# Kernel optimization log

Hardware: AMD Instinct MI355X
Metric: run time of the kernel (lower is better)

The kernel has to match this reference:

```python
import jax, jax.numpy as jnp
import numpy as np

H = 768   # hidden_size
E = 9     # num_entity_types
R = 10    # num_relation_types
B, S, N = 8, 4096, 64
P = N * (N - 1) // 2  # 2016 ordered pairs i<j


def setup_inputs() -> dict:
    key = jax.random.key(0)
    ks = jax.random.split(key, 10)
    sd = 0.02
    return {
        "sequence_output": jax.random.normal(ks[0], (B, S, H), jnp.float32),
        "attention_mask": jnp.ones((B, S), jnp.int32),
        "entity_spans": jnp.sort(jax.random.randint(ks[1], (B, N, 2), 0, S), axis=-1),
        # entity_classifier: Linear(H, H//2) -> ReLU -> Linear(H//2, E)
        "w1": jax.random.normal(ks[2], (H, H // 2), jnp.float32) * sd,
        "b1": jnp.zeros((H // 2,), jnp.float32),
        "w2": jax.random.normal(ks[3], (H // 2, E), jnp.float32) * sd,
        "b2": jnp.zeros((E,), jnp.float32),
        # relation_classifier: Linear(2H, H) -> ReLU -> Linear(H, R)
        "rw1": jax.random.normal(ks[4], (2 * H, H), jnp.float32) * sd,
        "rb1": jnp.zeros((H,), jnp.float32),
        "rw2": jax.random.normal(ks[5], (H, R), jnp.float32) * sd,
        "rb2": jnp.zeros((R,), jnp.float32),
    }


def reference(sequence_output, attention_mask, entity_spans,
              w1, b1, w2, b2, rw1, rb1, rw2, rb2):
    # entity classifier over all tokens (dropout is identity in eval)
    h = jax.nn.relu(jnp.einsum('bsh,hf->bsf', sequence_output, w1) + b1)
    entity_logits = jnp.einsum('bsf,fe->bse', h, w2) + b2  # [B,S,E]

    # span mean-pooling via a [B,N,S] membership mask (segment-mean)
    pos = jnp.arange(S)
    start = entity_spans[..., 0:1]  # [B,N,1]
    end = entity_spans[..., 1:2]    # [B,N,1]
    mask = ((pos >= start) & (pos < end)).astype(sequence_output.dtype)  # [B,N,S]
    counts = jnp.clip(mask.sum(-1, keepdims=True), 1.0)  # avoid /0 for empty spans
    entity_reprs = jnp.einsum('bns,bsh->bnh', mask, sequence_output) / counts  # [B,N,H]
    pooled_logits = jnp.einsum('bns,bse->bne', mask, entity_logits) / counts   # [B,N,E]
    entity_types = jnp.argmax(pooled_logits, axis=-1)  # [B,N]

    # all i<j pairs, batched relation classifier (replaces per-pair Python loop)
    ii, jj = np.triu_indices(N, k=1)  # static index sets, len P
    pair = jnp.concatenate([entity_reprs[:, ii], entity_reprs[:, jj]], axis=-1)  # [B,P,2H]
    rh = jax.nn.relu(jnp.einsum('bpk,kh->bph', pair, rw1) + rb1)
    relation_logits = jnp.einsum('bph,hr->bpr', rh, rw2) + rb2  # [B,P,R]
    relation_types = jnp.argmax(relation_logits, axis=-1)  # [B,P]

    return entity_logits, relation_logits, entity_reprs, entity_types, relation_types
```

## Files before the change

kernel.cpp:

```cpp
#include <hip/hip_runtime.h>
#include <hip/hip_bf16.h>

#define Hh 768
#define Ff 384
#define Ee 9
#define Rr 10
#define Bb 8
#define Ss 4096
#define Nn_ENT 64
#define Pp 2016
#define CH 16
#define NC 256

typedef short bf16x8 __attribute__((ext_vector_type(8)));
typedef float f32x4 __attribute__((ext_vector_type(4)));

__device__ __forceinline__ void async_copy16(void* lds, const void* g) {
  auto* l = (__attribute__((address_space(3))) unsigned int*)(lds);
  auto* p = (const __attribute__((address_space(1))) unsigned int*)(g);
  __builtin_amdgcn_global_load_lds(p, l, 16, 0, 0);
}

__global__ __launch_bounds__(256) void transpose_w1(const float* __restrict__ w1,
                                                    unsigned short* __restrict__ wt) {
  __shared__ unsigned short tile[64][65];
  const int bk = blockIdx.x * 64;
  const int bc = blockIdx.y * 64;
  const int c = threadIdx.x & 63, kq = threadIdx.x >> 6;
#pragma unroll
  for (int i = 0; i < 16; ++i) {
    int k = kq * 16 + i;
    float v = w1[(size_t)(bk + k) * Ff + bc + c];
    tile[c][k] = __bfloat16_as_ushort(__float2bfloat16(v));
  }
  __syncthreads();
  const int k2 = threadIdx.x & 63, cq = threadIdx.x >> 6;
#pragma unroll
  for (int i = 0; i < 16; ++i) {
    int c2 = cq * 16 + i;
    wt[(size_t)(bc + c2) * Hh + bk + k2] = tile[c2][k2];
  }
}

__global__ __launch_bounds__(192) void seq_prep(const float* __restrict__ seq,
                                                unsigned short* __restrict__ seq16,
                                                float* __restrict__ Pc) {
  const int c = blockIdx.x, b = blockIdx.y;
  const int t = threadIdx.x;
  const size_t base = ((size_t)b * Ss + (size_t)c * CH) * Hh;
  const float4* p = (const float4*)(seq + base) + t;
  ushort4* q = (ushort4*)(seq16 + base) + t;
  float4 acc = {0.f, 0.f, 0.f, 0.f};
#pragma unroll
  for (int s = 0; s < CH; ++s) {
    float4 v = p[(size_t)s * (Hh / 4)];
    acc.x += v.x; acc.y += v.y; acc.z += v.z; acc.w += v.w;
    ushort4 o;
    o.x = __bfloat16_as_ushort(__float2bfloat16(v.x));
    o.y = __bfloat16_as_ushort(__float2bfloat16(v.y));
    o.z = __bfloat16_as_ushort(__float2bfloat16(v.z));
    o.w = __bfloat16_as_ushort(__float2bfloat16(v.w));
    q[(size_t)s * (Hh / 4)] = o;
  }
  ((float4*)(Pc + ((size_t)b * NC + c) * Hh))[t] = acc;
}

__global__ __launch_bounds__(256) void gemm1_mfma(const unsigned short* __restrict__ A,
                                                  const unsigned short* __restrict__ Wt,
                                                  const float* __restrict__ b1,
                                                  unsigned short* __restrict__ H) {
  __shared__ unsigned short As[128 * 64];
  __shared__ unsigned short Bs[128 * 64];
  const int wg = blockIdx.x;
  const int lin = (wg & 7) * 96 + (wg >> 3);
  const int mt = lin / 3, nt = lin % 3;
  const int row0 = mt * 128, col0 = nt * 128;
  const int t = threadIdx.x;
  const int wid = t >> 6, lane = t & 63;
  const int wm = wid >> 1, wn = wid & 1;
  const int fr = lane & 15, fq = lane >> 4;
  const int srow = lane >> 3, scol = (lane & 7) * 8;
  const unsigned short* aA = A + (size_t)row0 * Hh;
  const unsigned short* aB = Wt + (size_t)col0 * Hh;

  f32x4 acc[4][4] = {};

  for (int ks = 0; ks < Hh / 64; ++ks) {
    const int k0 = ks * 64;
#pragma unroll
    for (int i = 0; i < 4; ++i) {
      const int r = (wid * 4 + i) * 8 + srow;
      async_copy16(&As[(wid * 4 + i) * 512], aA + (size_t)r * Hh + k0 + scol);
      async_copy16(&Bs[(wid * 4 + i) * 512], aB + (size_t)r * Hh + k0 + scol);
    }
    __syncthreads();
#pragma unroll
    for (int kk = 0; kk < 2; ++kk) {
      bf16x8 af[4], bfr[4];
#pragma unroll
      for (int m = 0; m < 4; ++m)
        af[m] = *(const bf16x8*)&As[(wm * 64 + m * 16 + fr) * 64 + kk * 32 + fq * 8];
#pragma unroll
      for (int n = 0; n < 4; ++n)
        bfr[n] = *(const bf16x8*)&Bs[(wn * 64 + n * 16 + fr) * 64 + kk * 32 + fq * 8];
#pragma unroll
      for (int m = 0; m < 4; ++m)
#pragma unroll
        for (int n = 0; n < 4; ++n)
          acc[m][n] = __builtin_amdgcn_mfma_f32_16x16x32_bf16(af[m], bfr[n], acc[m][n], 0, 0, 0);
    }
    if (ks < Hh / 64 - 1) __syncthreads();
  }

#pragma unroll
  for (int n = 0; n < 4; ++n) {
    const int col = col0 + wn * 64 + n * 16 + fr;
    const float bias = b1[col];
#pragma unroll
    for (int m = 0; m < 4; ++m) {
      const int rbase = row0 + wm * 64 + m * 16 + fq * 4;
#pragma unroll
      for (int j = 0; j < 4; ++j) {
        float x = fmaxf(acc[m][n][j] + bias, 0.f);
        H[(size_t)(rbase + j) * Ff + col] = __bfloat16_as_ushort(__float2bfloat16(x));
      }
    }
  }
}

__global__ __launch_bounds__(256) void gemm_uv_splitk(const float* __restrict__ A,
                                                      const float* __restrict__ rw1,
                                                      float* __restrict__ part) {
  const int uv = blockIdx.z & 1, ks = blockIdx.z >> 1;
  const float* Wp = rw1 + (size_t)uv * Hh * Hh + (size_t)ks * 192 * Hh;
  __shared__ float Ast[16][68];
  __shared__ float Wst[16][68];
  const int t = threadIdx.x;
  const int row0 = blockIdx.x * 64, col0 = blockIdx.y * 64;
  const int tm = (t & 15) * 4, tn = (t >> 4) * 4;
  const int lr = t >> 2, lk = (t & 3) * 4;
  const int wk = t >> 4, wc = (t & 15) * 4;
  float acc[4][4] = {};
  const float* Arow = A + (size_t)(row0 + lr) * Hh + ks * 192 + lk;
  for (int k0 = 0; k0 < 192; k0 += 16) {
    float4 av = *(const float4*)(Arow + k0);
    Ast[lk + 0][lr] = av.x; Ast[lk + 1][lr] = av.y;
    Ast[lk + 2][lr] = av.z; Ast[lk + 3][lr] = av.w;
    *(float4*)&Wst[wk][wc] = *(const float4*)(Wp + (size_t)(k0 + wk) * Hh + col0 + wc);
    __syncthreads();
#pragma unroll
    for (int kk = 0; kk < 16; ++kk) {
      const float4 a = *(const float4*)&Ast[kk][tm];
      const float4 b = *(const float4*)&Wst[kk][tn];
      acc[0][0] = fmaf(a.x, b.x, acc[0][0]); acc[0][1] = fmaf(a.x, b.y, acc[0][1]);
      acc[0][2] = fmaf(a.x, b.z, acc[0][2]); acc[0][3] = fmaf(a.x, b.w, acc[0][3]);
      acc[1][0] = fmaf(a.y, b.x, acc[1][0]); acc[1][1] = fmaf(a.y, b.y, acc[1][1]);
      acc[1][2] = fmaf(a.y, b.z, acc[1][2]); acc[1][3] = fmaf(a.y, b.w, acc[1][3]);
      acc[2][0] = fmaf(a.z, b.x, acc[2][0]); acc[2][1] = fmaf(a.z, b.y, acc[2][1]);
      acc[2][2] = fmaf(a.z, b.z, acc[2][2]); acc[2][3] = fmaf(a.z, b.w, acc[2][3]);
      acc[3][0] = fmaf(a.w, b.x, acc[3][0]); acc[3][1] = fmaf(a.w, b.y, acc[3][1]);
      acc[3][2] = fmaf(a.w, b.z, acc[3][2]); acc[3][3] = fmaf(a.w, b.w, acc[3][3]);
    }
    __syncthreads();
  }
  float* out = part + ((size_t)ks * 2 + uv) * (512 * Hh);
#pragma unroll
  for (int i = 0; i < 4; ++i) {
    float4 o; o.x = acc[i][0]; o.y = acc[i][1]; o.z = acc[i][2]; o.w = acc[i][3];
    *(float4*)(out + (size_t)(row0 + tm + i) * Hh + col0 + tn) = o;
  }
}

__global__ __launch_bounds__(256) void uv_reduce(const float* __restrict__ part,
                                                 float* __restrict__ uv) {
  const int i = blockIdx.x * 256 + threadIdx.x;
  const float4* p = (const float4*)part;
  float4 a = p[i], b = p[i + 196608], c = p[i + 2 * 196608], d = p[i + 3 * 196608];
  float4 o;
  o.x = (a.x + b.x) + (c.x + d.x);
  o.y = (a.y + b.y) + (c.y + d.y);
  o.z = (a.z + b.z) + (c.z + d.z);
  o.w = (a.w + b.w) + (c.w + d.w);
  ((float4*)uv)[i] = o;
}

__global__ __launch_bounds__(256) void gemm2_k(const __hip_bfloat16* __restrict__ h,
                                               const float* __restrict__ w2,
                                               const float* __restrict__ b2,
                                               float* __restrict__ out) {
  __shared__ float w2s[Ff * Ee];
  __shared__ float b2s[Ee];
  const int t = threadIdx.x;
  for (int i = t; i < Ff * Ee; i += 256) w2s[i] = w2[i];
  if (t < Ee) b2s[t] = b2[t];
  __syncthreads();
  const int lane = t & 63, warp = t >> 6;
  const int row = blockIdx.x * 64 + warp * 16 + (lane >> 2);
  const int q = lane & 3;
  float acc[Ee];
#pragma unroll
  for (int e = 0; e < Ee; ++e) acc[e] = 0.f;
  const unsigned short* hr = (const unsigned short*)h + (size_t)row * Ff;
  for (int k0 = q * 4; k0 < Ff; k0 += 16) {
    ushort4 us = *(const ushort4*)(hr + k0);
    float x0 = __uint_as_float((unsigned)us.x << 16);
    float x1 = __uint_as_float((unsigned)us.y << 16);
    float x2 = __uint_as_float((unsigned)us.z << 16);
    float x3 = __uint_as_float((unsigned)us.w << 16);
#pragma unroll
    for (int e = 0; e < Ee; ++e) {
      acc[e] = fmaf(x0, w2s[(k0 + 0) * Ee + e], acc[e]);
      acc[e] = fmaf(x1, w2s[(k0 + 1) * Ee + e], acc[e]);
      acc[e] = fmaf(x2, w2s[(k0 + 2) * Ee + e], acc[e]);
      acc[e] = fmaf(x3, w2s[(k0 + 3) * Ee + e], acc[e]);
    }
  }
#pragma unroll
  for (int e = 0; e < Ee; ++e) {
    acc[e] += __shfl_xor(acc[e], 1);
    acc[e] += __shfl_xor(acc[e], 2);
  }
  if (q == 0) {
#pragma unroll
    for (int e = 0; e < Ee; ++e) out[(size_t)row * Ee + e] = acc[e] + b2s[e];
  }
}

__global__ __launch_bounds__(256) void chunk_scan(float* __restrict__ Pc) {
  __shared__ float tile[NC][64];
  const int b = blockIdx.y;
  const int h0 = blockIdx.x * 64;
  float* base = Pc + (size_t)b * NC * Hh + h0;
  const int l = threadIdx.x & 63, g = threadIdx.x >> 6;
#pragma unroll 4
  for (int c = g * 64; c < g * 64 + 64; ++c)
    tile[c][l] = base[(size_t)c * Hh + l];
  __syncthreads();
  float run = 0.f;
#pragma unroll 4
  for (int c = g * 64; c < g * 64 + 64; ++c) {
    run += tile[c][l];
    tile[c][l] = run;
  }
  __syncthreads();
  float off = 0.f;
#pragma unroll
  for (int gg = 0; gg < 3; ++gg)
    if (gg < g) off += tile[gg * 64 + 63][l];
  __syncthreads();
  if (g > 0) {
#pragma unroll 4
    for (int c = g * 64; c < g * 64 + 64; ++c)
      tile[c][l] += off;
  }
  __syncthreads();
#pragma unroll 4
  for (int c = g * 64; c < g * 64 + 64; ++c)
    base[(size_t)c * Hh + l] = tile[c][l];
}

__global__ __launch_bounds__(192) void entity_reprs_k(const float* __restrict__ seq,
                                                      const float* __restrict__ Pc,
                                                      const int* __restrict__ spans,
                                                      float* __restrict__ reprs) {
  const int bn = blockIdx.x;
  const int b = bn >> 6;
  const int start = spans[bn * 2], end = spans[bn * 2 + 1];
  const int cnt = max(end - start, 1);
  const float inv = 1.0f / (float)cnt;
  const int cs = (start + CH - 1) >> 4, ce = end >> 4;
  const float* seqb = seq + (size_t)b * Ss * Hh;
  const float4* Pcb = (const float4*)(Pc + (size_t)b * NC * Hh);
  const int t = threadIdx.x;
  float4 acc = {0.f, 0.f, 0.f, 0.f};
  if (cs <= ce) {
    if (cs < ce) {
      float4 hi = Pcb[(size_t)(ce - 1) * 192 + t];
      acc.x += hi.x; acc.y += hi.y; acc.z += hi.z; acc.w += hi.w;
      if (cs > 0) {
        float4 lo = Pcb[(size_t)(cs - 1) * 192 + t];
        acc.x -= lo.x; acc.y -= lo.y; acc.z -= lo.z; acc.w -= lo.w;
      }
    }
    for (int s = start; s < cs * CH; ++s) {
      float4 v = ((const float4*)(seqb + (size_t)s * Hh))[t];
      acc.x += v.x; acc.y += v.y; acc.z += v.z; acc.w += v.w;
    }
    for (int s = ce * CH; s < end; ++s) {
      float4 v = ((const float4*)(seqb + (size_t)s * Hh))[t];
      acc.x += v.x; acc.y += v.y; acc.z += v.z; acc.w += v.w;
    }
  } else {
    for (int s = start; s < end; ++s) {
      float4 v = ((const float4*)(seqb + (size_t)s * Hh))[t];
      acc.x += v.x; acc.y += v.y; acc.z += v.z; acc.w += v.w;
    }
  }
  float4 o; o.x = acc.x * inv; o.y = acc.y * inv; o.z = acc.z * inv; o.w = acc.w * inv;
  ((float4*)(reprs + (size_t)bn * Hh))[t] = o;
}

__global__ __launch_bounds__(256) void pooled_argmax(const float* __restrict__ elog,
                                                     const int* __restrict__ spans,
                                                     float* __restrict__ etypes) {
  __shared__ float red[4][Ee];
  const int bn = blockIdx.x;
  const int b = bn >> 6;
  const int start = spans[bn * 2], end = spans[bn * 2 + 1];
  const int t = threadIdx.x, lane = t & 63, w = t >> 6;
  float acc[Ee];
#pragma unroll
  for (int e = 0; e < Ee; ++e) acc[e] = 0.f;
  const float* p = elog + (size_t)b * Ss * Ee;
  for (int s = start + t; s < end; s += 256) {
    const float* q = p + (size_t)s * Ee;
#pragma unroll
    for (int e = 0; e < Ee; ++e) acc[e] += q[e];
  }
#pragma unroll
  for (int off = 32; off; off >>= 1)
#pragma unroll
    for (int e = 0; e < Ee; ++e) acc[e] += __shfl_down(acc[e], off);
  if (lane == 0) {
#pragma unroll
    for (int e = 0; e < Ee; ++e) red[w][e] = acc[e];
  }
  __syncthreads();
  if (t == 0) {
    int best = 0; float bv = -1e30f;
#pragma unroll
    for (int e = 0; e < Ee; ++e) {
      float v = red[0][e] + red[1][e] + red[2][e] + red[3][e];
      if (v > bv) { bv = v; best = e; }
    }
    etypes[bn] = (float)best;
  }
}

__global__ __launch_bounds__(256) void relations_k(const float* __restrict__ UV,
                                                   const float* __restrict__ rb1,
                                                   const float* __restrict__ rw2,
                                                   const float* __restrict__ rb2,
                                                   float* __restrict__ rlogits,
                                                   float* __restrict__ rtypes) {
  const int p = blockIdx.x * 4 + (threadIdx.x >> 6);
  const int lane = threadIdx.x & 63;
  const int b = p / Pp, pp = p % Pp;
  int i = 0, off = 0;
  while (off + (Nn_ENT - 1 - i) <= pp) { off += Nn_ENT - 1 - i; ++i; }
  const int j = i + 1 + (pp - off);
  const float* u = UV + ((size_t)b * Nn_ENT + i) * Hh;
  const float* v = UV + (size_t)512 * Hh + ((size_t)b * Nn_ENT + j) * Hh;
  float acc[Rr];
#pragma unroll
  for (int r = 0; r < Rr; ++r) acc[r] = 0.f;
  for (int k = lane; k < Hh; k += 64) {
    float x = fmaxf(u[k] + v[k] + rb1[k], 0.f);
    const float* w = rw2 + (size_t)k * Rr;
#pragma unroll
    for (int r = 0; r < Rr; ++r) acc[r] = fmaf(x, w[r], acc[r]);
  }
#pragma unroll
  for (int off2 = 32; off2; off2 >>= 1)
#pragma unroll
    for (int r = 0; r < Rr; ++r) acc[r] += __shfl_down(acc[r], off2);
  if (lane == 0) {
    int best = 0; float bv = acc[0] + rb2[0];
    rlogits[(size_t)p * Rr + 0] = bv;
#pragma unroll
    for (int r = 1; r < Rr; ++r) {
      float val = acc[r] + rb2[r];
      rlogits[(size_t)p * Rr + r] = val;
      if (val > bv) { bv = val; best = r; }
    }
    rtypes[p] = (float)best;
  }
}

extern "C" void kernel_launch(void* const* d_in, const int* in_sizes, int n_in,
                              void* d_out, int out_size, void* d_ws, size_t ws_size,
                              hipStream_t stream) {
  const float* seq   = (const float*)d_in[0];
  const int*   spans = (const int*)d_in[2];
  const float* w1    = (const float*)d_in[3];
  const float* b1    = (const float*)d_in[4];
  const float* w2    = (const float*)d_in[5];
  const float* b2    = (const float*)d_in[6];
  const float* rw1   = (const float*)d_in[7];
  const float* rb1   = (const float*)d_in[8];
  const float* rw2   = (const float*)d_in[9];
  const float* rb2   = (const float*)d_in[10];

  float* out_elog = (float*)d_out;
  float* out_rlog = out_elog + 294912;
  float* out_repr = out_rlog + 161280;
  float* out_etyp = out_repr + 393216;
  float* out_rtyp = out_etyp + 512;

  unsigned short* ws_s16 = (unsigned short*)d_ws;
  __hip_bfloat16* ws_h   = (__hip_bfloat16*)((char*)d_ws + 50331648);
  float*          ws_pc  = (float*)((char*)d_ws + 75497472);
  float*          ws_uv  = (float*)((char*)d_ws + 81788928);
  unsigned short* ws_wt  = (unsigned short*)((char*)d_ws + 84934656);
  float*          ws_uvp = (float*)((char*)d_ws + 85524480);

  transpose_w1<<<dim3(12, 6), 256, 0, stream>>>(w1, ws_wt);
  seq_prep<<<dim3(NC, Bb), 192, 0, stream>>>(seq, ws_s16, ws_pc);
  gemm1_mfma<<<768, 256, 0, stream>>>(ws_s16, ws_wt, b1, (unsigned short*)ws_h);
  gemm2_k<<<512, 256, 0, stream>>>(ws_h, w2, b2, out_elog);
  chunk_scan<<<dim3(Hh / 64, Bb), 256, 0, stream>>>(ws_pc);
  entity_reprs_k<<<512, 192, 0, stream>>>(seq, ws_pc, spans, out_repr);
  gemm_uv_splitk<<<dim3(8, 12, 8), 256, 0, stream>>>(out_repr, rw1, ws_uvp);
  uv_reduce<<<768, 256, 0, stream>>>(ws_uvp, ws_uv);
  pooled_argmax<<<512, 256, 0, stream>>>(out_elog, spans, out_etyp);
  relations_k<<<4032, 256, 0, stream>>>(ws_uv, rb1, rw2, rb2, out_rlog, out_rtyp);
}
```

Before: 169.0 us.

## Fuse entity classifier second layer into the MFMA first-layer GEMM epilogue

The first-layer GEMM is retiled so each 512-thread block computes a full 64x384 row stripe. The ReLU hidden activations are then multiplied by w2 in registers and reduced through shuffles and LDS to produce entity logits directly. This removes the bf16 hidden buffer write and read and the separate gemm2 kernel launch. In exchange, each block reloads the whole W tile for every row stripe, LDS use per block grows, and the block count drops to 512.

```diff
diff --git a/kernel.cpp b/kernel.cpp
--- a/kernel.cpp
+++ b/kernel.cpp
@@ -65,66 +65,91 @@
   ((float4*)(Pc + ((size_t)b * NC + c) * Hh))[t] = acc;
 }
 
-__global__ __launch_bounds__(256) void gemm1_mfma(const unsigned short* __restrict__ A,
-                                                  const unsigned short* __restrict__ Wt,
-                                                  const float* __restrict__ b1,
-                                                  unsigned short* __restrict__ H) {
-  __shared__ unsigned short As[128 * 64];
-  __shared__ unsigned short Bs[128 * 64];
-  const int wg = blockIdx.x;
-  const int lin = (wg & 7) * 96 + (wg >> 3);
-  const int mt = lin / 3, nt = lin % 3;
-  const int row0 = mt * 128, col0 = nt * 128;
+__global__ __launch_bounds__(512, 4) void gemm1_fused(const unsigned short* __restrict__ A,
+                                                      const unsigned short* __restrict__ Wt,
+                                                      const float* __restrict__ b1,
+                                                      const float* __restrict__ w2,
+                                                      const float* __restrict__ b2,
+                                                      float* __restrict__ elog) {
+  __shared__ unsigned short AB[(64 + 384) * 64];
+  __shared__ float w2s[Ff * Ee];
+  __shared__ float b1s[Ff];
+  __shared__ float b2s[Ee];
+  unsigned short* As = AB;
+  unsigned short* Bs = AB + 64 * 64;
+  float* red = (float*)AB;
+
   const int t = threadIdx.x;
   const int wid = t >> 6, lane = t & 63;
-  const int wm = wid >> 1, wn = wid & 1;
+  const int wm = wid >> 2, wn = wid & 3;
   const int fr = lane & 15, fq = lane >> 4;
-  const int srow = lane >> 3, scol = (lane & 7) * 8;
-  const unsigned short* aA = A + (size_t)row0 * Hh;
-  const unsigned short* aB = Wt + (size_t)col0 * Hh;
-
-  f32x4 acc[4][4] = {};
+  const int row0 = blockIdx.x * 64;
+
+  for (int i = t; i < Ff * Ee; i += 512) w2s[i] = w2[i];
+  for (int i = t; i < Ff; i += 512) b1s[i] = b1[i];
+  if (t < Ee) b2s[t] = b2[t];
+
+  const unsigned short* aA = A + (size_t)(row0 + (t >> 3)) * Hh + (t & 7) * 8;
+  const unsigned short* aB = Wt + (size_t)(t >> 3) * Hh + (t & 7) * 8;
+
+  f32x4 acc[2][6] = {};
 
   for (int ks = 0; ks < Hh / 64; ++ks) {
     const int k0 = ks * 64;
-#pragma unroll
-    for (int i = 0; i < 4; ++i) {
-      const int r = (wid * 4 + i) * 8 + srow;
-      async_copy16(&As[(wid * 4 + i) * 512], aA + (size_t)r * Hh + k0 + scol);
-      async_copy16(&Bs[(wid * 4 + i) * 512], aB + (size_t)r * Hh + k0 + scol);
-    }
+    async_copy16(&As[wid * 512], aA + k0);
+#pragma unroll
+    for (int i = 0; i < 6; ++i)
+      async_copy16(&Bs[i * 4096 + wid * 512], aB + (size_t)i * 64 * Hh + k0);
     __syncthreads();
 #pragma unroll
     for (int kk = 0; kk < 2; ++kk) {
-      bf16x8 af[4], bfr[4];
-#pragma unroll
-      for (int m = 0; m < 4; ++m)
-        af[m] = *(const bf16x8*)&As[(wm * 64 + m * 16 + fr) * 64 + kk * 32 + fq * 8];
-#pragma unroll
-      for (int n = 0; n < 4; ++n)
-        bfr[n] = *(const bf16x8*)&Bs[(wn * 64 + n * 16 + fr) * 64 + kk * 32 + fq * 8];
-#pragma unroll
-      for (int m = 0; m < 4; ++m)
-#pragma unroll
-        for (int n = 0; n < 4; ++n)
+      bf16x8 af[2], bfr[6];
+#pragma unroll
+      for (int m = 0; m < 2; ++m)
+        af[m] = *(const bf16x8*)&As[(wm * 32 + m * 16 + fr) * 64 + kk * 32 + fq * 8];
+#pragma unroll
+      for (int n = 0; n < 6; ++n)
+        bfr[n] = *(const bf16x8*)&Bs[(wn * 96 + n * 16 + fr) * 64 + kk * 32 + fq * 8];
+#pragma unroll
+      for (int m = 0; m < 2; ++m)
+#pragma unroll
+        for (int n = 0; n < 6; ++n)
           acc[m][n] = __builtin_amdgcn_mfma_f32_16x16x32_bf16(af[m], bfr[n], acc[m][n], 0, 0, 0);
     }
-    if (ks < Hh / 64 - 1) __syncthreads();
-  }
-
-#pragma unroll
-  for (int n = 0; n < 4; ++n) {
-    const int col = col0 + wn * 64 + n * 16 + fr;
-    const float bias = b1[col];
-#pragma unroll
-    for (int m = 0; m < 4; ++m) {
-      const int rbase = row0 + wm * 64 + m * 16 + fq * 4;
-#pragma unroll
-      for (int j = 0; j < 4; ++j) {
-        float x = fmaxf(acc[m][n][j] + bias, 0.f);
-        H[(size_t)(rbase + j) * Ff + col] = __bfloat16_as_ushort(__float2bfloat16(x));
+    __syncthreads();
+  }
+
+#pragma unroll
+  for (int m = 0; m < 2; ++m) {
+#pragma unroll
+    for (int j = 0; j < 4; ++j) {
+      float p[Ee];
+#pragma unroll
+      for (int e = 0; e < Ee; ++e) p[e] = 0.f;
+#pragma unroll
+      for (int n = 0; n < 6; ++n) {
+        const int col = wn * 96 + n * 16 + fr;
+        const float hv = fmaxf(acc[m][n][j] + b1s[col], 0.f);
+        const float* wrow = &w2s[col * Ee];
+#pragma unroll
+        for (int e = 0; e < Ee; ++e) p[e] = fmaf(hv, wrow[e], p[e]);
       }
-    }
+#pragma unroll
+      for (int mask = 1; mask <= 8; mask <<= 1)
+#pragma unroll
+        for (int e = 0; e < Ee; ++e) p[e] += __shfl_xor(p[e], mask);
+      if (fr < Ee) {
+        const int row = wm * 32 + m * 16 + fq * 4 + j;
+        red[(wn * 64 + row) * Ee + fr] = p[fr];
+      }
+    }
+  }
+  __syncthreads();
+  for (int idx = t; idx < 64 * Ee; idx += 512) {
+    const int row = idx / Ee, e = idx - row * Ee;
+    float v = red[(0 * 64 + row) * Ee + e] + red[(1 * 64 + row) * Ee + e]
+            + red[(2 * 64 + row) * Ee + e] + red[(3 * 64 + row) * Ee + e] + b2s[e];
+    elog[(size_t)(row0 + row) * Ee + e] = v;
   }
 }
 
@@ -182,48 +207,6 @@
   o.z = (a.z + b.z) + (c.z + d.z);
   o.w = (a.w + b.w) + (c.w + d.w);
   ((float4*)uv)[i] = o;
-}
-
-__global__ __launch_bounds__(256) void gemm2_k(const __hip_bfloat16* __restrict__ h,
-                                               const float* __restrict__ w2,
-                                               const float* __restrict__ b2,
-                                               float* __restrict__ out) {
-  __shared__ float w2s[Ff * Ee];
-  __shared__ float b2s[Ee];
-  const int t = threadIdx.x;
-  for (int i = t; i < Ff * Ee; i += 256) w2s[i] = w2[i];
-  if (t < Ee) b2s[t] = b2[t];
-  __syncthreads();
-  const int lane = t & 63, warp = t >> 6;
-  const int row = blockIdx.x * 64 + warp * 16 + (lane >> 2);
-  const int q = lane & 3;
-  float acc[Ee];
-#pragma unroll
-  for (int e = 0; e < Ee; ++e) acc[e] = 0.f;
-  const unsigned short* hr = (const unsigned short*)h + (size_t)row * Ff;
-  for (int k0 = q * 4; k0 < Ff; k0 += 16) {
-    ushort4 us = *(const ushort4*)(hr + k0);
-    float x0 = __uint_as_float((unsigned)us.x << 16);
-    float x1 = __uint_as_float((unsigned)us.y << 16);
-    float x2 = __uint_as_float((unsigned)us.z << 16);
-    float x3 = __uint_as_float((unsigned)us.w << 16);
-#pragma unroll
-    for (int e = 0; e < Ee; ++e) {
-      acc[e] = fmaf(x0, w2s[(k0 + 0) * Ee + e], acc[e]);
-      acc[e] = fmaf(x1, w2s[(k0 + 1) * Ee + e], acc[e]);
-      acc[e] = fmaf(x2, w2s[(k0 + 2) * Ee + e], acc[e]);
-      acc[e] = fmaf(x3, w2s[(k0 + 3) * Ee + e], acc[e]);
-    }
-  }
-#pragma unroll
-  for (int e = 0; e < Ee; ++e) {
-    acc[e] += __shfl_xor(acc[e], 1);
-    acc[e] += __shfl_xor(acc[e], 2);
-  }
-  if (q == 0) {
-#pragma unroll
-    for (int e = 0; e < Ee; ++e) out[(size_t)row * Ee + e] = acc[e] + b2s[e];
-  }
 }
 
 __global__ __launch_bounds__(256) void chunk_scan(float* __restrict__ Pc) {
@@ -398,16 +381,14 @@
   float* out_rtyp = out_etyp + 512;
 
   unsigned short* ws_s16 = (unsigned short*)d_ws;
-  __hip_bfloat16* ws_h   = (__hip_bfloat16*)((char*)d_ws + 50331648);
-  float*          ws_pc  = (float*)((char*)d_ws + 75497472);
-  float*          ws_uv  = (float*)((char*)d_ws + 81788928);
-  unsigned short* ws_wt  = (unsigned short*)((char*)d_ws + 84934656);
-  float*          ws_uvp = (float*)((char*)d_ws + 85524480);
+  float*          ws_pc  = (float*)((char*)d_ws + 50331648);
+  float*          ws_uv  = (float*)((char*)d_ws + 56623104);
+  unsigned short* ws_wt  = (unsigned short*)((char*)d_ws + 59768832);
+  float*          ws_uvp = (float*)((char*)d_ws + 60358656);
 
   transpose_w1<<<dim3(12, 6), 256, 0, stream>>>(w1, ws_wt);
   seq_prep<<<dim3(NC, Bb), 192, 0, stream>>>(seq, ws_s16, ws_pc);
-  gemm1_mfma<<<768, 256, 0, stream>>>(ws_s16, ws_wt, b1, (unsigned short*)ws_h);
-  gemm2_k<<<512, 256, 0, stream>>>(ws_h, w2, b2, out_elog);
+  gemm1_fused<<<512, 512, 0, stream>>>(ws_s16, ws_wt, b1, w2, b2, out_elog);
   chunk_scan<<<dim3(Hh / 64, Bb), 256, 0, stream>>>(ws_pc);
   entity_reprs_k<<<512, 192, 0, stream>>>(seq, ws_pc, spans, out_repr);
   gemm_uv_splitk<<<dim3(8, 12, 8), 256, 0, stream>>>(out_repr, rw1, ws_uvp);
```

After: 164.5 us. -2.7%, faster.
